# Optimization experiments

Measured on AMD Instinct MI355X. Metric: run time of the kernel, lower is better.

The kernel has to match this reference:

```python
import jax, jax.numpy as jnp
import numpy as np

FILTERS = 512
DQK = FILTERS // 8  # 64


def setup_inputs() -> dict:
    key = jax.random.key(0)
    ks = jax.random.split(key, 7)
    B, H, W, C = 32, 32, 32, FILTERS
    x = jax.random.normal(ks[0], (B, H, W, C), dtype=jnp.float32)
    # 1x1 convs == per-pixel dense layers: weight [Cin, Cout], bias [Cout]
    def glorot(k, cin, cout):
        lim = np.sqrt(6.0 / (cin + cout)).astype(np.float32)
        return jax.random.uniform(k, (cin, cout), jnp.float32, -lim, lim)
    return {
        "x": x,
        "wq": glorot(ks[1], C, DQK), "bq": jnp.zeros((DQK,), jnp.float32),
        "wk": glorot(ks[2], C, DQK), "bk": jnp.zeros((DQK,), jnp.float32),
        "wv": glorot(ks[3], C, C),   "bv": jnp.zeros((C,), jnp.float32),
    }


def reference(x, wq, bq, wk, bk, wv, bv):
    B, H, W, C = x.shape
    N = H * W
    xf = x.reshape(B, N, C)                       # flatten spatial -> tokens
    q = xf @ wq + bq                              # [B, N, C//8]
    k = xf @ wk + bk                              # [B, N, C//8]
    v = xf @ wv + bv                              # [B, N, C]
    scale = 1.0 / jnp.sqrt(jnp.float32(C // 8))
    scores = jnp.einsum('bnd,bmd->bnm', q, k) * scale  # [B, N, N]
    probs = jax.nn.softmax(scores, axis=-1)
    attended = jnp.einsum('bnm,bmc->bnc', probs, v)    # [B, N, C]
    return attended.reshape(B, H, W, C) + x
```

## Files before the change

### kernel.cpp

```cpp
#include <hip/hip_runtime.h>
#include <stdint.h>

#define B_ 32
#define N_ 1024
#define C_ 512
#define D_ 64

typedef __attribute__((ext_vector_type(8))) __bf16 bf8;
typedef __attribute__((ext_vector_type(4))) float f32x4;
typedef __attribute__((ext_vector_type(8))) unsigned short u16x8;

typedef const __attribute__((address_space(1))) void* gp_t;
typedef __attribute__((address_space(3))) void* lp_t;

__device__ inline void g2l16(const void* g, void* l) {
    __builtin_amdgcn_global_load_lds((gp_t)g, (lp_t)l, 16, 0, 0);
}

__device__ inline float b2f(unsigned short u) {
    return __uint_as_float(((unsigned)u) << 16);
}
__device__ inline unsigned short f2b(float f) {
    unsigned u = __float_as_uint(f);
    u += 0x7FFF + ((u >> 16) & 1);
    return (unsigned short)(u >> 16);
}

#define MFMA16(a, b, c) __builtin_amdgcn_mfma_f32_16x16x32_bf16((a), (b), (c), 0, 0, 0)

__global__ __launch_bounds__(256) void xcvt(const float* __restrict__ x,
                                            unsigned short* __restrict__ xb) {
    int i = blockIdx.x * 256 + threadIdx.x;
    float4 f = ((const float4*)x)[i];
    ushort4 o;
    o.x = f2b(f.x); o.y = f2b(f.y); o.z = f2b(f.z); o.w = f2b(f.w);
    ((ushort4*)xb)[i] = o;
}

__global__ __launch_bounds__(256) void wtrans(const float* __restrict__ w,
                                              unsigned short* __restrict__ wt,
                                              int cout) {
    int t = blockIdx.x * 256 + threadIdx.x;
    int co = t >> 9;
    int ci = t & 511;
    wt[t] = f2b(w[(size_t)ci * cout + co]);
}

__global__ __launch_bounds__(256) void qkv(
    const unsigned short* __restrict__ xb,
    const unsigned short* __restrict__ WT,
    const float* __restrict__ bq, const float* __restrict__ bk,
    const float* __restrict__ bv,
    unsigned short* __restrict__ q, unsigned short* __restrict__ k,
    unsigned short* __restrict__ vT)
{
    const int L = blockIdx.x;
    const int s = L >> 3;
    const int rb = (L & 7) + 8 * (s / 5);
    const int cb = s % 5;
    const int tid = threadIdx.x;
    const int lane = tid & 63;
    const int wave = tid >> 6;
    const int wm = wave >> 1, wn = wave & 1;
    const int lr = lane & 15;
    const int lk = lane >> 4;

    __shared__ unsigned short SM[16896];
    unsigned short* As = SM;
    unsigned short* Bs = SM + 8192;
    unsigned short* TB = SM;

    const int row0 = rb * 128;
    const int col0 = cb * 128;

    f32x4 zero4 = {0.f, 0.f, 0.f, 0.f};
    f32x4 acc[4][4];
    #pragma unroll
    for (int i = 0; i < 4; ++i)
        #pragma unroll
        for (int j = 0; j < 4; ++j) acc[i][j] = zero4;

    for (int kk = 0; kk < C_; kk += 64) {
        __syncthreads();
        #pragma unroll
        for (int i = 0; i < 4; ++i) {
            int f = wave * 4 + i;
            int t = f >> 1, kq = f & 1;
            g2l16(xb + (size_t)(row0 + t * 16 + lr) * C_ + kk + kq * 32 + lk * 8,
                  &As[f * 512]);
            g2l16(WT + (size_t)(col0 + t * 16 + lr) * C_ + kk + kq * 32 + lk * 8,
                  &Bs[f * 512]);
        }
        __syncthreads();
        #pragma unroll
        for (int kq = 0; kq < 2; ++kq) {
            bf8 a[4], bb[4];
            #pragma unroll
            for (int ti = 0; ti < 4; ++ti)
                a[ti] = *(const bf8*)&As[((wm * 4 + ti) * 2 + kq) * 512 + lane * 8];
            #pragma unroll
            for (int tj = 0; tj < 4; ++tj)
                bb[tj] = *(const bf8*)&Bs[((wn * 4 + tj) * 2 + kq) * 512 + lane * 8];
            #pragma unroll
            for (int ti = 0; ti < 4; ++ti)
                #pragma unroll
                for (int tj = 0; tj < 4; ++tj)
                    acc[ti][tj] = MFMA16(a[ti], bb[tj], acc[ti][tj]);
        }
    }

    if (cb == 0) {
        unsigned short* outp = (wn == 0) ? q : k;
        const float* bias = (wn == 0) ? bq : bk;
        #pragma unroll
        for (int ti = 0; ti < 4; ++ti)
            #pragma unroll
            for (int tj = 0; tj < 4; ++tj) {
                int col = tj * 16 + lr;
                float bi = bias[col];
                #pragma unroll
                for (int r = 0; r < 4; ++r) {
                    int row = row0 + wm * 64 + ti * 16 + lk * 4 + r;
                    outp[(size_t)row * D_ + col] = f2b(acc[ti][tj][r] + bi);
                }
            }
    } else {
        const int colv = (cb - 1) * 128;
        __syncthreads();
        #pragma unroll
        for (int ti = 0; ti < 4; ++ti)
            #pragma unroll
            for (int tj = 0; tj < 4; ++tj) {
                int c = wn * 64 + tj * 16 + lr;
                float bi = bv[colv + c];
                int tok = wm * 64 + ti * 16 + lk * 4;
                ushort4 o;
                o.x = f2b(acc[ti][tj][0] + bi);
                o.y = f2b(acc[ti][tj][1] + bi);
                o.z = f2b(acc[ti][tj][2] + bi);
                o.w = f2b(acc[ti][tj][3] + bi);
                *(ushort4*)&TB[c * 132 + tok] = o;
            }
        __syncthreads();
        const int b  = row0 >> 10;
        const int n0 = row0 & 1023;
        #pragma unroll
        for (int i = 0; i < 16; ++i) {
            int idx = tid + 256 * i;
            int c = idx >> 5, ch = idx & 31;
            ushort4 t4 = *(const ushort4*)&TB[c * 132 + ch * 4];
            *(ushort4*)&vT[((size_t)(b * C_ + colv + c)) * N_ + n0 + ch * 4] = t4;
        }
    }
}

#define SLD 1032
__global__ __launch_bounds__(256) void attn(
    const unsigned short* __restrict__ q,
    const unsigned short* __restrict__ k,
    const unsigned short* __restrict__ vT,
    const float* __restrict__ x,
    float* __restrict__ out)
{
    const int bid = blockIdx.x;
    const int b   = (bid & 7) + 8 * (bid >> 8);
    const int qt  = (bid >> 3) & 31;
    const int n0  = qt * 32;
    const int tid = threadIdx.x, lane = tid & 63, wave = tid >> 6;
    const int lr = lane & 15, lk = lane >> 4;

    __shared__ unsigned short S[32 * SLD];
    __shared__ float inv_s[32];

    bf8 qa[2][2];
    #pragma unroll
    for (int rt = 0; rt < 2; ++rt)
        #pragma unroll
        for (int kq = 0; kq < 2; ++kq)
            qa[rt][kq] = *(const bf8*)&q[(size_t)(b * N_ + n0 + rt * 16 + lr) * D_
                                         + kq * 32 + lk * 8];

    const int m0w = wave * 256;
    #pragma unroll 2
    for (int mt2 = 0; mt2 < 8; ++mt2) {
        #pragma unroll
        for (int h = 0; h < 2; ++h) {
            int m = m0w + mt2 * 32 + h * 16;
            const unsigned short* kp = k + (size_t)(b * N_ + m + lr) * D_ + lk * 8;
            bf8 kb0 = *(const bf8*)(kp);
            bf8 kb1 = *(const bf8*)(kp + 32);
            #pragma unroll
            for (int rt = 0; rt < 2; ++rt) {
                f32x4 s4 = {0.f, 0.f, 0.f, 0.f};
                s4 = MFMA16(qa[rt][0], kb0, s4);
                s4 = MFMA16(qa[rt][1], kb1, s4);
                #pragma unroll
                for (int r = 0; r < 4; ++r)
                    S[(rt * 16 + lk * 4 + r) * SLD + m + lr] = f2b(s4[r] * 0.125f);
            }
        }
    }
    __syncthreads();

    #pragma unroll
    for (int i = 0; i < 8; ++i) {
        int row = wave * 8 + i;
        u16x8 a = *(const u16x8*)&S[row * SLD + lane * 16];
        u16x8 c = *(const u16x8*)&S[row * SLD + lane * 16 + 8];
        float v[16];
        #pragma unroll
        for (int j = 0; j < 8; ++j) { v[j] = b2f(a[j]); v[8 + j] = b2f(c[j]); }
        float mx = v[0];
        #pragma unroll
        for (int j = 1; j < 16; ++j) mx = fmaxf(mx, v[j]);
        #pragma unroll
        for (int off = 32; off; off >>= 1) mx = fmaxf(mx, __shfl_xor(mx, off));
        float sum = 0.f;
        #pragma unroll
        for (int j = 0; j < 16; ++j) { v[j] = __expf(v[j] - mx); sum += v[j]; }
        #pragma unroll
        for (int off = 32; off; off >>= 1) sum += __shfl_xor(sum, off);
        u16x8 oa, oc;
        #pragma unroll
        for (int j = 0; j < 8; ++j) { oa[j] = f2b(v[j]); oc[j] = f2b(v[8 + j]); }
        *(u16x8*)&S[row * SLD + lane * 16] = oa;
        *(u16x8*)&S[row * SLD + lane * 16 + 8] = oc;
        if (lane == 0) inv_s[row] = 1.f / sum;
    }
    __syncthreads();

    const int cbase = wave * 128;
    f32x4 zero4 = {0.f, 0.f, 0.f, 0.f};
    f32x4 acc[8][2];
    #pragma unroll
    for (int ct = 0; ct < 8; ++ct) { acc[ct][0] = zero4; acc[ct][1] = zero4; }

    const unsigned short* Vb = vT + ((size_t)b * C_ + cbase) * N_;
    #pragma unroll 2
    for (int mt = 0; mt < 32; ++mt) {
        const int m0 = mt * 32;
        bf8 va[8];
        #pragma unroll
        for (int ct = 0; ct < 8; ++ct)
            va[ct] = *(const bf8*)&Vb[(size_t)(ct * 16 + lr) * N_ + m0 + lk * 8];
        bf8 pb0 = *(const bf8*)&S[lr * SLD + m0 + lk * 8];
        bf8 pb1 = *(const bf8*)&S[(16 + lr) * SLD + m0 + lk * 8];
        #pragma unroll
        for (int ct = 0; ct < 8; ++ct) {
            acc[ct][0] = MFMA16(va[ct], pb0, acc[ct][0]);
            acc[ct][1] = MFMA16(va[ct], pb1, acc[ct][1]);
        }
    }

    #pragma unroll
    for (int rt = 0; rt < 2; ++rt) {
        float invr = inv_s[rt * 16 + lr];
        #pragma unroll
        for (int ct = 0; ct < 8; ++ct) {
            size_t base = (size_t)(b * N_ + n0 + rt * 16 + lr) * C_
                        + cbase + ct * 16 + lk * 4;
            float4 xr = *(const float4*)&x[base];
            float4 o;
            o.x = acc[ct][rt][0] * invr + xr.x;
            o.y = acc[ct][rt][1] * invr + xr.y;
            o.z = acc[ct][rt][2] * invr + xr.z;
            o.w = acc[ct][rt][3] * invr + xr.w;
            *(float4*)&out[base] = o;
        }
    }
}

extern "C" void kernel_launch(void* const* d_in, const int* in_sizes, int n_in,
                              void* d_out, int out_size, void* d_ws, size_t ws_size,
                              hipStream_t stream) {
    (void)in_sizes; (void)n_in; (void)out_size; (void)ws_size;
    const float* xf = (const float*)d_in[0];
    const float* wq = (const float*)d_in[1];
    const float* bq = (const float*)d_in[2];
    const float* wk = (const float*)d_in[3];
    const float* bk = (const float*)d_in[4];
    const float* wv = (const float*)d_in[5];
    const float* bv = (const float*)d_in[6];
    float* out = (float*)d_out;

    char* ws = (char*)d_ws;
    unsigned short* qb  = (unsigned short*)(ws);
    unsigned short* kb  = (unsigned short*)(ws + 4194304);
    unsigned short* vTb = (unsigned short*)(ws + 8388608);
    unsigned short* WT  = (unsigned short*)(ws + 41943040);
    unsigned short* xb  = (unsigned short*)(ws + 42598400);

    xcvt<<<16384, 256, 0, stream>>>(xf, xb);
    wtrans<<<128, 256, 0, stream>>>(wq, WT, 64);
    wtrans<<<128, 256, 0, stream>>>(wk, WT + 64 * 512, 64);
    wtrans<<<1024, 256, 0, stream>>>(wv, WT + 128 * 512, 512);
    qkv<<<1280, 256, 0, stream>>>(xb, WT, bq, bk, bv, qb, kb, vTb);
    attn<<<1024, 256, 0, stream>>>(qb, kb, vTb, xf, out);
}
```

Baseline: 327.3 us.

## Split attention score tile into two online-softmax halves with swizzled LDS

The attention kernel now processes the 1024 keys in two 512-wide halves, using an online softmax (running max, sum and rescale factor per row) so the shared score buffer shrinks from about 66KB to 32KB. An XOR swizzle on the LDS index replaces row padding to avoid bank conflicts, and launch bounds request 4 blocks per CU to raise occupancy. The V loads are split into groups of four to reduce register pressure. In exchange it adds extra barriers, per-half accumulator rescaling, and a sequential dependency between the halves.

Result: slower. 369.2 us (+12.8%).

```diff
diff --git a/kernel.cpp b/kernel.cpp
--- a/kernel.cpp
+++ b/kernel.cpp
@@ -154,8 +154,12 @@
     }
 }
 
-#define SLD 1032
-__global__ __launch_bounds__(256) void attn(
+#define TM 512
+__device__ inline int sidx(int row, int chunk) {
+    return row * TM + ((chunk ^ (row & 7)) << 3);
+}
+
+__global__ __launch_bounds__(256, 4) void attn(
     const unsigned short* __restrict__ q,
     const unsigned short* __restrict__ k,
     const unsigned short* __restrict__ vT,
@@ -169,8 +173,10 @@
     const int tid = threadIdx.x, lane = tid & 63, wave = tid >> 6;
     const int lr = lane & 15, lk = lane >> 4;
 
-    __shared__ unsigned short S[32 * SLD];
-    __shared__ float inv_s[32];
+    __shared__ unsigned short S[32 * TM];
+    __shared__ float m_s[32], l_s[32], alpha_s[32];
+
+    if (tid < 32) { m_s[tid] = -1e30f; l_s[tid] = 0.f; }
 
     bf8 qa[2][2];
     #pragma unroll
@@ -180,13 +186,22 @@
             qa[rt][kq] = *(const bf8*)&q[(size_t)(b * N_ + n0 + rt * 16 + lr) * D_
                                          + kq * 32 + lk * 8];
 
-    const int m0w = wave * 256;
-    #pragma unroll 2
-    for (int mt2 = 0; mt2 < 8; ++mt2) {
-        #pragma unroll
-        for (int h = 0; h < 2; ++h) {
-            int m = m0w + mt2 * 32 + h * 16;
-            const unsigned short* kp = k + (size_t)(b * N_ + m + lr) * D_ + lk * 8;
+    f32x4 zero4 = {0.f, 0.f, 0.f, 0.f};
+    f32x4 acc[8][2];
+    #pragma unroll
+    for (int ct = 0; ct < 8; ++ct) { acc[ct][0] = zero4; acc[ct][1] = zero4; }
+
+    const int m0w = wave * 128;
+    const int cbase = wave * 128;
+
+    for (int h = 0; h < 2; ++h) {
+        const int mb = h * TM;
+        if (h) __syncthreads();
+
+        #pragma unroll 2
+        for (int mt = 0; mt < 8; ++mt) {
+            int ml = m0w + mt * 16;
+            const unsigned short* kp = k + (size_t)(b * N_ + mb + ml + lr) * D_ + lk * 8;
             bf8 kb0 = *(const bf8*)(kp);
             bf8 kb1 = *(const bf8*)(kp + 32);
             #pragma unroll
@@ -195,66 +210,81 @@
                 s4 = MFMA16(qa[rt][0], kb0, s4);
                 s4 = MFMA16(qa[rt][1], kb1, s4);
                 #pragma unroll
-                for (int r = 0; r < 4; ++r)
-                    S[(rt * 16 + lk * 4 + r) * SLD + m + lr] = f2b(s4[r] * 0.125f);
+                for (int r = 0; r < 4; ++r) {
+                    int row = rt * 16 + lk * 4 + r;
+                    int col = ml + lr;
+                    S[sidx(row, col >> 3) + (col & 7)] = f2b(s4[r] * 0.125f);
+                }
+            }
+        }
+        __syncthreads();
+
+        #pragma unroll
+        for (int i = 0; i < 8; ++i) {
+            int row = wave * 8 + i;
+            u16x8 a = *(const u16x8*)&S[sidx(row, lane)];
+            float v[8];
+            #pragma unroll
+            for (int j = 0; j < 8; ++j) v[j] = b2f(a[j]);
+            float tmax = v[0];
+            #pragma unroll
+            for (int j = 1; j < 8; ++j) tmax = fmaxf(tmax, v[j]);
+            #pragma unroll
+            for (int off = 32; off; off >>= 1) tmax = fmaxf(tmax, __shfl_xor(tmax, off));
+            float mold = m_s[row];
+            float mnew = fmaxf(mold, tmax);
+            float sum = 0.f;
+            #pragma unroll
+            for (int j = 0; j < 8; ++j) { v[j] = __expf(v[j] - mnew); sum += v[j]; }
+            #pragma unroll
+            for (int off = 32; off; off >>= 1) sum += __shfl_xor(sum, off);
+            u16x8 o;
+            #pragma unroll
+            for (int j = 0; j < 8; ++j) o[j] = f2b(v[j]);
+            *(u16x8*)&S[sidx(row, lane)] = o;
+            if (lane == 0) {
+                float al = __expf(mold - mnew);
+                alpha_s[row] = al;
+                m_s[row] = mnew;
+                l_s[row] = l_s[row] * al + sum;
+            }
+        }
+        __syncthreads();
+
+        float a0 = alpha_s[lr], a1 = alpha_s[16 + lr];
+        #pragma unroll
+        for (int ct = 0; ct < 8; ++ct) {
+            #pragma unroll
+            for (int r = 0; r < 4; ++r) { acc[ct][0][r] *= a0; acc[ct][1][r] *= a1; }
+        }
+        const unsigned short* Vb = vT + ((size_t)b * C_ + cbase) * N_ + mb;
+        #pragma unroll 2
+        for (int mt = 0; mt < 16; ++mt) {
+            int ml = mt * 32;
+            bf8 pb0 = *(const bf8*)&S[sidx(lr,      (ml >> 3) + lk)];
+            bf8 pb1 = *(const bf8*)&S[sidx(16 + lr, (ml >> 3) + lk)];
+            #pragma unroll
+            for (int g = 0; g < 2; ++g) {
+                bf8 va[4];
+                #pragma unroll
+                for (int cc = 0; cc < 4; ++cc) {
+                    int ct = g * 4 + cc;
+                    va[cc] = *(const bf8*)&Vb[(size_t)(ct * 16 + lr) * N_ + ml + lk * 8];
+                }
+                #pragma unroll
+                for (int cc = 0; cc < 4; ++cc) {
+                    int ct = g * 4 + cc;
+                    acc[ct][0] = MFMA16(va[cc], pb0, acc[ct][0]);
+                    acc[ct][1] = MFMA16(va[cc], pb1, acc[ct][1]);
+                }
             }
         }
     }
-    __syncthreads();
-
-    #pragma unroll
-    for (int i = 0; i < 8; ++i) {
-        int row = wave * 8 + i;
-        u16x8 a = *(const u16x8*)&S[row * SLD + lane * 16];
-        u16x8 c = *(const u16x8*)&S[row * SLD + lane * 16 + 8];
-        float v[16];
-        #pragma unroll
-        for (int j = 0; j < 8; ++j) { v[j] = b2f(a[j]); v[8 + j] = b2f(c[j]); }
-        float mx = v[0];
-        #pragma unroll
-        for (int j = 1; j < 16; ++j) mx = fmaxf(mx, v[j]);
-        #pragma unroll
-        for (int off = 32; off; off >>= 1) mx = fmaxf(mx, __shfl_xor(mx, off));
-        float sum = 0.f;
-        #pragma unroll
-        for (int j = 0; j < 16; ++j) { v[j] = __expf(v[j] - mx); sum += v[j]; }
-        #pragma unroll
-        for (int off = 32; off; off >>= 1) sum += __shfl_xor(sum, off);
-        u16x8 oa, oc;
-        #pragma unroll
-        for (int j = 0; j < 8; ++j) { oa[j] = f2b(v[j]); oc[j] = f2b(v[8 + j]); }
-        *(u16x8*)&S[row * SLD + lane * 16] = oa;
-        *(u16x8*)&S[row * SLD + lane * 16 + 8] = oc;
-        if (lane == 0) inv_s[row] = 1.f / sum;
-    }
-    __syncthreads();
-
-    const int cbase = wave * 128;
-    f32x4 zero4 = {0.f, 0.f, 0.f, 0.f};
-    f32x4 acc[8][2];
-    #pragma unroll
-    for (int ct = 0; ct < 8; ++ct) { acc[ct][0] = zero4; acc[ct][1] = zero4; }
-
-    const unsigned short* Vb = vT + ((size_t)b * C_ + cbase) * N_;
-    #pragma unroll 2
-    for (int mt = 0; mt < 32; ++mt) {
-        const int m0 = mt * 32;
-        bf8 va[8];
-        #pragma unroll
-        for (int ct = 0; ct < 8; ++ct)
-            va[ct] = *(const bf8*)&Vb[(size_t)(ct * 16 + lr) * N_ + m0 + lk * 8];
-        bf8 pb0 = *(const bf8*)&S[lr * SLD + m0 + lk * 8];
-        bf8 pb1 = *(const bf8*)&S[(16 + lr) * SLD + m0 + lk * 8];
-        #pragma unroll
-        for (int ct = 0; ct < 8; ++ct) {
-            acc[ct][0] = MFMA16(va[ct], pb0, acc[ct][0]);
-            acc[ct][1] = MFMA16(va[ct], pb1, acc[ct][1]);
-        }
-    }
-
+
+    float i0 = 1.f / l_s[lr], i1 = 1.f / l_s[16 + lr];
     #pragma unroll
     for (int rt = 0; rt < 2; ++rt) {
-        float invr = inv_s[rt * 16 + lr];
+        float invr = rt ? i1 : i0;
         #pragma unroll
         for (int ct = 0; ct < 8; ++ct) {
             size_t base = (size_t)(b * N_ + n0 + rt * 16 + lr) * C_
```
